# Kernel tuning notes

Hardware: AMD Instinct MI355X
Metric: run time of the kernel (lower is better)

Reference implementation:

```python
import jax, jax.numpy as jnp
import numpy as np
from jax import lax

B, S, F, I, D, K, V = 8, 4096, 256, 512, 4, 7, 256  # batch, seq, features, intermediate, depth, kernel, classes


def setup_inputs() -> dict:
    key = jax.random.key(0)
    ks = jax.random.split(key, 7)

    def nrm(k, shape, fan_in):
        return jax.random.normal(k, shape, jnp.float32) / np.float32(np.sqrt(fan_in))

    return {
        "inp": jax.random.randint(ks[0], (B, S), 0, V),
        "emb": nrm(ks[1], (V, 2 * F), F),
        "w0": nrm(ks[2], (D, 3 * I, F, 1), F),          # 1x1 gating conv, features -> 3*intermediate
        "w1": nrm(ks[3], (D, 3 * I, I, K), I * K),       # causal conv, intermediate -> 3*intermediate
        "w2": nrm(ks[4], (D, F, I, 1), I),               # 1x1 conv, intermediate -> features
        "out_w": nrm(ks[5], (V, 2 * F, 1), 2 * F),
        "out_b": jnp.zeros((V,), jnp.float32),
    }


def mish(x):
    return x * jnp.tanh(jax.nn.softplus(x))


def conv1x1(x, w):
    # x: [B, C, S], w: [O, C, 1] -> [B, O, S]
    return jnp.einsum('bcs,oc->bos', x, w[..., 0])


def causal_conv(x, w):
    # x: [B, C, S], w: [O, C, K]; left-pad with K-1 zeros for causality
    k = w.shape[-1]
    xp = jnp.pad(x, ((0, 0), (0, 0), (k - 1, 0)))
    return lax.conv_general_dilated(xp, w, (1,), 'VALID',
                                    dimension_numbers=('NCH', 'OIH', 'NCH'))


def lin_attn(v, divisor):
    # v: [B, 3I, S]; cumsum-normalized linear attention: cumsum(depth)/t * scale + shift
    depth, scale, shift = jnp.split(v, 3, axis=1)
    return jnp.cumsum(depth, axis=-1) / divisor * scale + shift


def cell(x, w0, w1, w2, divisor):
    v = lin_attn(mish(conv1x1(x, w0)), divisor)     # [B, I, S]
    v = lin_attn(mish(causal_conv(v, w1)), divisor) # [B, I, S]
    return conv1x1(v, w2)                            # [B, F, S]


def reference(inp, emb, w0, w1, w2, out_w, out_b):
    divisor = jnp.arange(1, S + 1, dtype=jnp.float32)[None, None, :]  # [1,1,S]
    e = jnp.transpose(emb[inp], (0, 2, 1))  # [B, 2F, S]
    x0, x1 = jnp.split(e, 2, axis=1)
    # reversible residual stack: (x0, x1) -> (x1, x0 + cell(x1))
    for d in range(D):
        x0, x1 = x1, x0 + cell(x1, w0[d], w1[d], w2[d], divisor)
    out = jnp.concatenate([x0, x1], axis=1)  # [B, 2F, S]
    return conv1x1(out, out_w) + out_b[None, :, None]  # [B, V, S]
```

## Files before the change

kernel.cpp:

```cpp
#include <hip/hip_runtime.h>
#include <hip/hip_bf16.h>

#define B_ 8
#define S_ 4096
#define F_ 256
#define I_ 512
#define D_ 4
#define K_ 7
#define V_ 256
#define I3_ 1536
#define KE_ 3584
#define VR_ (S_ + 8)

using bf16 = __hip_bfloat16;
typedef __bf16 bf16x8 __attribute__((ext_vector_type(8)));
typedef float  f32x4  __attribute__((ext_vector_type(4)));

#define LDS_PTR(p) ((__attribute__((address_space(3))) void*)(p))
#define GLB_PTR(p) ((const __attribute__((address_space(1))) void*)(p))

#define BARR_()  __builtin_amdgcn_s_barrier()
#define WLGKM_() asm volatile("s_waitcnt lgkmcnt(0)" ::: "memory")
#define WVM0_()  asm volatile("s_waitcnt vmcnt(0)" ::: "memory")

__device__ __forceinline__ float mishf(float x) {
    float u = expf(fminf(x, 30.0f));
    float t = u * (u + 2.0f);
    return x * (t / (t + 2.0f));
}

__device__ __forceinline__ float loadw(const void* p, size_t i, int isbf) {
    return isbf ? __bfloat162float(((const bf16*)p)[i]) : ((const float*)p)[i];
}

__device__ __forceinline__ __bf16 tobf(float x) {
    bf16 h = __float2bfloat16(x);
    return *(__bf16*)&h;
}

__global__ __launch_bounds__(256)
void detect_kernel(int* __restrict__ flag, const unsigned short* __restrict__ p)
{
    __shared__ int sh[256];
    int cnt = 0;
    for (int j = threadIdx.x; j < 16384; j += 256) {
        unsigned int e = (p[j] >> 7) & 0xffu;
        if (e >= 132u) cnt++;
    }
    sh[threadIdx.x] = cnt;
    __syncthreads();
    for (int s = 128; s > 0; s >>= 1) {
        if ((int)threadIdx.x < s) sh[threadIdx.x] += sh[threadIdx.x + s];
        __syncthreads();
    }
    if (threadIdx.x == 0) flag[0] = (sh[0] == 0) ? 1 : 0;
}

__global__ __launch_bounds__(256)
void embed_kernel(float* __restrict__ x0, float* __restrict__ x1,
                  const int* __restrict__ inp, const void* __restrict__ emb,
                  const int* __restrict__ flag)
{
    const int isbf = flag[0];
    size_t idx = (size_t)blockIdx.x * 256 + threadIdx.x;
    int s = (int)(idx % S_);
    int f = (int)((idx / S_) % F_);
    int b = (int)(idx / ((size_t)S_ * F_));
    int tok = inp[b * S_ + s];
    x0[idx] = loadw(emb, (size_t)tok * (2 * F_) + f, isbf);
    x1[idx] = loadw(emb, (size_t)tok * (2 * F_) + F_ + f, isbf);
}

__global__ __launch_bounds__(256)
void zeropad_kernel(bf16* __restrict__ vbt, int nslice)
{
    int i = blockIdx.x * 256 + threadIdx.x;
    if (i < nslice * 6 * I_) {
        int z = i / (6 * I_), off = i % (6 * I_);
        vbt[(size_t)z * VR_ * I_ + off] = __float2bfloat16(0.0f);
    }
}

__global__ __launch_bounds__(256)
void wprep_kernel(bf16* __restrict__ wexp, bf16* __restrict__ wb0,
                  bf16* __restrict__ wb2, const void* __restrict__ w1,
                  const void* __restrict__ w0, const void* __restrict__ w2,
                  size_t o1w, size_t o0w, size_t o2w, const int* __restrict__ flag)
{
    const int isbf = flag[0];
    int idx = blockIdx.x * 256 + threadIdx.x;
    if (idx < I3_ * I_) {
        int c = idx & 511, o = idx >> 9;
        const size_t base = o1w + ((size_t)o * 512 + c) * 7;
        float vals[7];
        #pragma unroll
        for (int k = 0; k < 7; ++k) vals[k] = loadw(w1, base + k, isbf);
        #pragma unroll
        for (int k = 0; k < 7; ++k)
            wexp[(size_t)o * KE_ + (k << 9) + c] = __float2bfloat16(vals[k]);
    } else if (idx < I3_ * I_ + I3_ * F_) {
        int i = idx - I3_ * I_;
        wb0[i] = __float2bfloat16(loadw(w0, o0w + i, isbf));
    } else if (idx < I3_ * I_ + I3_ * F_ + F_ * I_) {
        int i = idx - I3_ * I_ - I3_ * F_;
        wb2[i] = __float2bfloat16(loadw(w2, o2w + i, isbf));
    }
}

__global__ __launch_bounds__(256)
void scan_kernel(bf16* __restrict__ vout, const float* __restrict__ t)
{
    const int z = blockIdx.y;
    const int i = blockIdx.x;
    t    += (size_t)z * I3_ * S_;
    vout += (size_t)z * I_ * S_;
    const float* dp  = t + (size_t)i * S_;
    const float* scp = dp + (size_t)I_ * S_;
    const float* shp = dp + (size_t)(2 * I_) * S_;
    bf16* op = vout + (size_t)i * S_;
    const int tid = threadIdx.x;
    const int base = tid * 16;

    float md[16];
    float lsum = 0.f;
    #pragma unroll
    for (int q = 0; q < 4; ++q) {
        float4 dv = *(const float4*)(dp + base + q * 4);
        #pragma unroll
        for (int j = 0; j < 4; ++j) {
            float m = (&dv.x)[j];
            md[q * 4 + j] = m;
            lsum += m;
        }
    }
    float ssum = lsum;
    #pragma unroll
    for (int off = 1; off < 64; off <<= 1) {
        float nv = __shfl_up(ssum, off, 64);
        if ((tid & 63) >= off) ssum += nv;
    }
    __shared__ float wtot[4];
    const int wid = tid >> 6, lane = tid & 63;
    if (lane == 63) wtot[wid] = ssum;
    __syncthreads();
    float excl = ssum - lsum;
    #pragma unroll
    for (int wq = 0; wq < 3; ++wq)
        if (wq < wid) excl += wtot[wq];

    float run = excl;
    bf16x8 o0v, o1v;
    #pragma unroll
    for (int q = 0; q < 4; ++q) {
        float4 scv = *(const float4*)(scp + base + q * 4);
        float4 shv = *(const float4*)(shp + base + q * 4);
        #pragma unroll
        for (int j = 0; j < 4; ++j) {
            run += md[q * 4 + j];
            float sdiv = (float)(base + q * 4 + j + 1);
            float ov = run / sdiv * (&scv.x)[j] + (&shv.x)[j];
            if (q < 2) o0v[q * 4 + j] = tobf(ov);
            else       o1v[(q - 2) * 4 + j] = tobf(ov);
        }
    }
    *(bf16x8*)(void*)(op + base) = o0v;
    *(bf16x8*)(void*)(op + base + 8) = o1v;
}

__global__ __launch_bounds__(256)
void trans_kernel(bf16* __restrict__ dst, size_t dzstr,
                  const float* __restrict__ src, size_t szstr, int C)
{
    __shared__ __align__(16) bf16 lt[64][72];
    const int z = blockIdx.z;
    dst += (size_t)z * dzstr;
    src += (size_t)z * szstr;
    const int tid = threadIdx.x;
    const int s0 = blockIdx.x * 64;
    const int c0 = blockIdx.y * 64;
    #pragma unroll
    for (int p = 0; p < 4; ++p) {
        int c = p * 16 + (tid >> 4);
        int sc = (tid & 15) * 4;
        float4 f = *(const float4*)(src + (size_t)(c0 + c) * S_ + s0 + sc);
        #pragma unroll
        for (int j = 0; j < 4; ++j)
            lt[sc + j][c] = __float2bfloat16((&f.x)[j]);
    }
    __syncthreads();
    #pragma unroll
    for (int p = 0; p < 2; ++p) {
        int ch = p * 256 + tid;
        int r = ch >> 3, g = ch & 7;
        *(bf16x8*)(dst + (size_t)(s0 + r) * C + c0 + g * 8) =
            *(const bf16x8*)&lt[r][g * 8];
    }
}

__global__ __launch_bounds__(256)
void transb_kernel(bf16* __restrict__ dst, size_t dzstr,
                   const bf16* __restrict__ src, size_t szstr, int C)
{
    __shared__ __align__(16) bf16 lt[64][72];
    const int z = blockIdx.z;
    dst += (size_t)z * dzstr;
    src += (size_t)z * szstr;
    const int tid = threadIdx.x;
    const int s0 = blockIdx.x * 64;
    const int c0 = blockIdx.y * 64;
    #pragma unroll
    for (int p = 0; p < 2; ++p) {
        int c = p * 32 + (tid >> 3);
        int sc = (tid & 7) * 8;
        bf16x8 v = *(const bf16x8*)(src + (size_t)(c0 + c) * S_ + s0 + sc);
        #pragma unroll
        for (int j = 0; j < 8; ++j)
            *(__bf16*)&lt[sc + j][c] = v[j];
    }
    __syncthreads();
    #pragma unroll
    for (int p = 0; p < 2; ++p) {
        int ch = p * 256 + tid;
        int r = ch >> 3, g = ch & 7;
        *(bf16x8*)(dst + (size_t)(s0 + r) * C + c0 + g * 8) =
            *(const bf16x8*)&lt[r][g * 8];
    }
}

__global__ __launch_bounds__(512, 1)
void gemm192_kernel(float* __restrict__ out, size_t ozstr,
                    const bf16* __restrict__ Aw, int lda,
                    const bf16* __restrict__ Bm, size_t bzstr, int ldb,
                    int Kdim, int conv, int domish)
{
    __shared__ __align__(16) bf16 la[2][192][64];
    __shared__ __align__(16) bf16 lb[2][256][64];
    const int tid = threadIdx.x;
    const int s0 = blockIdx.x * 256;
    const int o0 = blockIdx.y * 192;
    const int z  = blockIdx.z;
    out += (size_t)z * ozstr;
    Bm  += (size_t)z * bzstr;
    const int wv = tid >> 6, lane = tid & 63;
    const int wr = wv >> 2, wc = wv & 3;
    const int l16 = lane & 15, q = lane >> 4;
    const int srow = lane >> 3;
    const int schunk = (lane & 7) ^ srow;
    const int nKt = Kdim >> 6;

    f32x4 acc[6][4];
    #pragma unroll
    for (int i = 0; i < 6; ++i)
        #pragma unroll
        for (int j = 0; j < 4; ++j)
            #pragma unroll
            for (int r = 0; r < 4; ++r) acc[i][j][r] = 0.f;

#define STAGE_A3(buf, kt) do {                                                \
    const bf16* gpA_ = Aw + (size_t)(o0 + wv * 8 + srow) * lda                \
                          + ((kt) << 6) + (schunk << 3);                      \
    __builtin_amdgcn_global_load_lds(GLB_PTR(gpA_),                           \
        LDS_PTR(&la[buf][wv * 8][0]), 16, 0, 0);                              \
    __builtin_amdgcn_global_load_lds(GLB_PTR(gpA_ + (size_t)64 * lda),        \
        LDS_PTR(&la[buf][64 + wv * 8][0]), 16, 0, 0);                         \
    __builtin_amdgcn_global_load_lds(GLB_PTR(gpA_ + (size_t)128 * lda),       \
        LDS_PTR(&la[buf][128 + wv * 8][0]), 16, 0, 0);                        \
} while (0)

#define STAGE_BL(buf, l, ro, bk) do {                                         \
    const bf16* gpB_ = Bm + (size_t)(s0 + (l) * 64 + wv * 8 + srow + (ro)) * ldb \
                          + (bk) + (schunk << 3);                             \
    __builtin_amdgcn_global_load_lds(GLB_PTR(gpB_),                           \
        LDS_PTR(&lb[buf][(l) * 64 + wv * 8][0]), 16, 0, 0);                   \
} while (0)

#define LDAF6(buf, kk) do {                                                   \
    _Pragma("unroll") for (int i2 = 0; i2 < 6; ++i2) {                        \
        int r_ = wr * 96 + i2 * 16 + l16;                                     \
        af[i2] = *(const bf16x8*)&la[buf][r_][(((kk) * 4 + q) ^ (r_ & 7)) << 3]; \
    }                                                                         \
} while (0)

#define LDBF4(buf, kk) do {                                                   \
    _Pragma("unroll") for (int j2 = 0; j2 < 4; ++j2) {                        \
        int r_ = wc * 64 + j2 * 16 + l16;                                     \
        bfr[j2] = *(const bf16x8*)&lb[buf][r_][(((kk) * 4 + q) ^ (r_ & 7)) << 3]; \
    }                                                                         \
} while (0)

#define MFMA24() do {                                                         \
    __builtin_amdgcn_s_setprio(1);                                            \
    _Pragma("unroll") for (int i2 = 0; i2 < 6; ++i2)                          \
    _Pragma("unroll") for (int j2 = 0; j2 < 4; ++j2)                          \
        acc[i2][j2] = __builtin_amdgcn_mfma_f32_16x16x32_bf16(                \
            af[i2], bfr[j2], acc[i2][j2], 0, 0, 0);                           \
    __builtin_amdgcn_s_setprio(0);                                            \
} while (0)

    STAGE_A3(0, 0);
    STAGE_BL(0, 0, 0, 0); STAGE_BL(0, 1, 0, 0);
    STAGE_BL(0, 2, 0, 0); STAGE_BL(0, 3, 0, 0);
    WVM0_();
    BARR_();

    bf16x8 af[6], bfr[4];
    for (int t = 0; t < nKt; ++t) {
        const int c = t & 1, n = c ^ 1;
        const bool st = (t + 1) < nKt;
        int ro1 = 0, bk1 = (t + 1) << 6;
        if (conv) { ro1 = bk1 >> 9; bk1 &= 511; }
        LDAF6(c, 0); LDBF4(c, 0);
        if (st) {
            STAGE_A3(n, t + 1);
            STAGE_BL(n, 0, ro1, bk1); STAGE_BL(n, 1, ro1, bk1);
            STAGE_BL(n, 2, ro1, bk1); STAGE_BL(n, 3, ro1, bk1);
        }
        BARR_(); WLGKM_();
        MFMA24();
        LDAF6(c, 1); LDBF4(c, 1);
        if (st) WVM0_();
        BARR_(); WLGKM_();
        MFMA24();
    }

    #pragma unroll
    for (int i = 0; i < 6; ++i)
        #pragma unroll
        for (int j = 0; j < 4; ++j) {
            int sg = s0 + wc * 64 + j * 16 + l16;
            #pragma unroll
            for (int r = 0; r < 4; ++r) {
                int og = o0 + wr * 96 + i * 16 + q * 4 + r;
                float v = acc[i][j][r];
                if (domish) v = mishf(v);
                out[(size_t)og * S_ + sg] = v;
            }
        }
#undef STAGE_A3
#undef STAGE_BL
#undef LDAF6
#undef LDBF4
#undef MFMA24
}

__global__ __launch_bounds__(256)
void gemm128_kernel(float* __restrict__ out, size_t ozstr,
                    const bf16* __restrict__ Aw, int lda,
                    const bf16* __restrict__ Bm, size_t bzstr, int ldb,
                    int Kdim, int conv, int addres)
{
    __shared__ __align__(16) bf16 la[2][128][64];
    __shared__ __align__(16) bf16 lb[2][128][64];
    const int tid = threadIdx.x;
    const int s0 = blockIdx.x * 128;
    const int o0 = blockIdx.y * 128;
    const int z  = blockIdx.z;
    out += (size_t)z * ozstr;
    Bm  += (size_t)z * bzstr;
    const int wv = tid >> 6, lane = tid & 63;
    const int wo = wv & 1, wsv = wv >> 1;
    const int l16 = lane & 15, q = lane >> 4;
    const int lrow = lane >> 3, lslot = lane & 7;
    const int nKt = Kdim >> 6;

    f32x4 acc[4][4];
    #pragma unroll
    for (int i = 0; i < 4; ++i)
        #pragma unroll
        for (int j = 0; j < 4; ++j)
            #pragma unroll
            for (int r = 0; r < 4; ++r) acc[i][j][r] = 0.f;

#define G128_STAGE(buf, kt) do {                                              \
    int k0_ = (kt) << 6; int roff_ = 0, bk_ = k0_;                            \
    if (conv) { roff_ = k0_ >> 9; bk_ = k0_ & 511; }                          \
    _Pragma("unroll") for (int t_ = 0; t_ < 4; ++t_) {                        \
        int rbase = wv * 32 + t_ * 8;                                         \
        int row = rbase + lrow;                                               \
        int chunk = lslot ^ (row & 7);                                        \
        __builtin_amdgcn_global_load_lds(                                     \
            GLB_PTR(Aw + (size_t)(o0 + row) * lda + k0_ + chunk * 8),         \
            LDS_PTR(&la[buf][rbase][0]), 16, 0, 0);                           \
        __builtin_amdgcn_global_load_lds(                                     \
            GLB_PTR(Bm + (size_t)(s0 + row + roff_) * ldb + bk_ + chunk * 8), \
            LDS_PTR(&lb[buf][rbase][0]), 16, 0, 0);                           \
    }                                                                         \
} while (0)

#define G128_RD(buf, kk) do {                                                 \
    _Pragma("unroll") for (int i = 0; i < 4; ++i) {                           \
        int r = wo * 64 + i * 16 + l16;                                       \
        af[i] = *(const bf16x8*)&la[buf][r][(((kk) * 4 + q) ^ (r & 7)) * 8];  \
    }                                                                         \
    _Pragma("unroll") for (int j = 0; j < 4; ++j) {                           \
        int r = wsv * 64 + j * 16 + l16;                                      \
        bfr[j] = *(const bf16x8*)&lb[buf][r][(((kk) * 4 + q) ^ (r & 7)) * 8]; \
    }                                                                         \
} while (0)

#define G128_MFMA16() do {                                                    \
    __builtin_amdgcn_s_setprio(1);                                            \
    _Pragma("unroll") for (int i = 0; i < 4; ++i)                             \
    _Pragma("unroll") for (int j = 0; j < 4; ++j)                             \
        acc[i][j] = __builtin_amdgcn_mfma_f32_16x16x32_bf16(                  \
            af[i], bfr[j], acc[i][j], 0, 0, 0);                               \
    __builtin_amdgcn_s_setprio(0);                                            \
} while (0)

    G128_STAGE(0, 0);
    WVM0_();
    BARR_();

    bf16x8 af[4], bfr[4];
    for (int t = 0; t < nKt; ++t) {
        const int c = t & 1, n = c ^ 1;
        const bool st = (t + 1) < nKt;
        G128_RD(c, 0);
        if (st) G128_STAGE(n, t + 1);
        BARR_(); WLGKM_();
        G128_MFMA16();
        G128_RD(c, 1);
        if (st) WVM0_();
        BARR_(); WLGKM_();
        G128_MFMA16();
    }

    #pragma unroll
    for (int i = 0; i < 4; ++i)
        #pragma unroll
        for (int j = 0; j < 4; ++j) {
            int sg = s0 + wsv * 64 + j * 16 + l16;
            #pragma unroll
            for (int r = 0; r < 4; ++r) {
                int og = o0 + wo * 64 + i * 16 + q * 4 + r;
                float v = acc[i][j][r];
                if (addres) v += out[(size_t)og * S_ + sg];
                out[(size_t)og * S_ + sg] = v;
            }
        }
#undef G128_STAGE
#undef G128_RD
#undef G128_MFMA16
}

__global__ __launch_bounds__(256)
void final_kernel(void* __restrict__ out, const float* __restrict__ x0,
                  const float* __restrict__ x1, const void* __restrict__ ow,
                  const void* __restrict__ ob, const int* __restrict__ flag)
{
    __shared__ float wl[16][68];
    __shared__ float xl[16][68];
    const int isbf = flag[0];
    const int tid = threadIdx.x;
    const int tx = tid & 15, ty = tid >> 4;
    const int s0 = blockIdx.x * 64;
    const int o0 = blockIdx.y * 64;
    const int b  = blockIdx.z;
    float acc[4][4] = {};
    for (int c0 = 0; c0 < 2 * F_; c0 += 16) {
        if (isbf) {
            #pragma unroll
            for (int e = tid; e < 1024; e += 256) {
                int k = e & 15, o = e >> 4;
                wl[k][o] = __bfloat162float(((const bf16*)ow)[(size_t)(o0 + o) * (2 * F_) + (c0 + k)]);
            }
        } else {
            #pragma unroll
            for (int e = tid; e < 1024; e += 256) {
                int k = e & 15, o = e >> 4;
                wl[k][o] = ((const float*)ow)[(size_t)(o0 + o) * (2 * F_) + (c0 + k)];
            }
        }
        {
            int r = tid >> 4;
            int qq = (tid & 15) * 4;
            int cr = c0 + r;
            const float* src = (cr < F_) ? (x0 + ((size_t)b * F_ + cr) * S_)
                                         : (x1 + ((size_t)b * F_ + (cr - F_)) * S_);
            *(float4*)&xl[r][qq] = *(const float4*)(src + s0 + qq);
        }
        __syncthreads();
        #pragma unroll
        for (int k = 0; k < 16; ++k) {
            float4 av = *(const float4*)&wl[k][ty * 4];
            float4 bv = *(const float4*)&xl[k][tx * 4];
            #pragma unroll
            for (int i = 0; i < 4; ++i)
                #pragma unroll
                for (int j = 0; j < 4; ++j)
                    acc[i][j] += (&av.x)[i] * (&bv.x)[j];
        }
        __syncthreads();
    }
    #pragma unroll
    for (int i = 0; i < 4; ++i) {
        int o = o0 + ty * 4 + i;
        float bias = loadw(ob, o, isbf);
        size_t outoff = ((size_t)b * V_ + o) * S_ + s0 + tx * 4;
        if (isbf) {
            bf16* po = (bf16*)out + outoff;
            #pragma unroll
            for (int j = 0; j < 4; ++j)
                po[j] = __float2bfloat16(acc[i][j] + bias);
        } else {
            float* po = (float*)out + outoff;
            *(float4*)po = make_float4(acc[i][0] + bias, acc[i][1] + bias,
                                       acc[i][2] + bias, acc[i][3] + bias);
        }
    }
}

extern "C" void kernel_launch(void* const* d_in, const int* in_sizes, int n_in,
                              void* d_out, int out_size, void* d_ws, size_t ws_size,
                              hipStream_t stream)
{
    const int*  inp  = (const int*)d_in[0];
    const void* emb  = d_in[1];
    const void* w0   = d_in[2];
    const void* w1   = d_in[3];
    const void* w2   = d_in[4];
    const void* outw = d_in[5];
    const void* outb = d_in[6];

    const size_t NX = (size_t)B_ * F_ * S_;
    const size_t NT = (size_t)I3_ * S_;
    const size_t NV = (size_t)I_ * S_;
    const size_t VSTR = (size_t)VR_ * I_;

    auto need = [&](int p) -> size_t {
        return 256 + 8 * NX + (size_t)4 * p * NT + (size_t)2 * p * NV
             + 2 * ((size_t)I3_ * KE_ + (size_t)p * VSTR + (size_t)p * S_ * F_
                    + (size_t)I3_ * F_ + (size_t)F_ * I_);
    };
    int P = 2;
    if (ws_size >= need(8)) P = 8;
    else if (ws_size >= need(4)) P = 4;

    int*   flag = (int*)d_ws;
    float* A  = (float*)d_ws + 64;
    float* Bb = A + NX;
    float* T  = Bb + NX;
    bf16*  Vv = (bf16*)(T + (size_t)P * NT);
    bf16*  wexp = Vv + (size_t)P * NV;
    bf16*  vbt  = wexp + (size_t)I3_ * KE_;
    bf16*  xbt  = vbt + (size_t)P * VSTR;
    bf16*  wb0  = xbt + (size_t)P * S_ * F_;
    bf16*  wb2  = wb0 + (size_t)I3_ * F_;

    detect_kernel<<<1, 256, 0, stream>>>(flag, (const unsigned short*)emb);
    embed_kernel<<<dim3((unsigned)(NX / 256)), 256, 0, stream>>>(A, Bb, inp, emb, flag);
    zeropad_kernel<<<dim3((P * 6 * I_ + 255) / 256), 256, 0, stream>>>(vbt, P);

    const unsigned WPREP_GRID = (I3_ * I_ + I3_ * F_ + F_ * I_ + 255) / 256;
    int swap = 0;
    for (int d = 0; d < D_; ++d) {
        wprep_kernel<<<dim3(WPREP_GRID), 256, 0, stream>>>(
            wexp, wb0, wb2, w1, w0, w2,
            (size_t)d * I3_ * I_ * K_, (size_t)d * I3_ * F_,
            (size_t)d * F_ * I_, flag);
        for (int bp = 0; bp < B_ / P; ++bp) {
            float* x0 = (swap ? Bb : A) + (size_t)(P * bp) * F_ * S_;
            float* x1 = (swap ? A : Bb) + (size_t)(P * bp) * F_ * S_;
            trans_kernel<<<dim3(S_ / 64, F_ / 64, P), 256, 0, stream>>>(
                xbt, (size_t)S_ * F_, x1, (size_t)F_ * S_, F_);
            gemm192_kernel<<<dim3(S_ / 256, I3_ / 192, P), 512, 0, stream>>>(
                T, NT, wb0, F_, xbt, (size_t)S_ * F_, F_, F_, 0, 1);
            scan_kernel<<<dim3(I_, P), 256, 0, stream>>>(Vv, T);
            transb_kernel<<<dim3(S_ / 64, I_ / 64, P), 256, 0, stream>>>(
                vbt + 6 * I_, VSTR, Vv, NV, I_);
            gemm192_kernel<<<dim3(S_ / 256, I3_ / 192, P), 512, 0, stream>>>(
                T, NT, wexp, KE_, vbt, VSTR, I_, KE_, 1, 1);
            scan_kernel<<<dim3(I_, P), 256, 0, stream>>>(Vv, T);
            transb_kernel<<<dim3(S_ / 64, I_ / 64, P), 256, 0, stream>>>(
                vbt + 6 * I_, VSTR, Vv, NV, I_);
            gemm128_kernel<<<dim3(S_ / 128, F_ / 128, P), 256, 0, stream>>>(
                x0, (size_t)F_ * S_, wb2, I_, vbt + 6 * I_, VSTR, I_, I_, 0, 1);
        }
        swap ^= 1;
    }
    final_kernel<<<dim3(S_ / 64, V_ / 64, B_), 256, 0, stream>>>(d_out, A, Bb, outw, outb, flag);
    (void)in_sizes; (void)n_in; (void)out_size;
}
```

Measured before the change: 2.649 ms.

## Store scale/shift intermediates in bf16 and add 256-row GEMM tile for batch-8

The gating GEMMs now write the depth third of their output in fp32 and the scale and shift thirds in bf16, so the scan kernel reads less intermediate data. A new gemm256 kernel with a 256x256 tile is used when all 8 batches fit in the workspace, giving more reuse per block and fewer blocks. Rounding scale and shift to bf16 adds small precision loss, and the larger tile raises register and LDS pressure.

```diff
diff --git a/kernel.cpp b/kernel.cpp
--- a/kernel.cpp
+++ b/kernel.cpp
@@ -38,6 +38,12 @@
     return *(__bf16*)&h;
 }
 
+__device__ __forceinline__ float bf2f(__bf16 h) {
+    unsigned short u = __builtin_bit_cast(unsigned short, h);
+    unsigned int x = (unsigned int)u << 16;
+    return __builtin_bit_cast(float, x);
+}
+
 __global__ __launch_bounds__(256)
 void detect_kernel(int* __restrict__ flag, const unsigned short* __restrict__ p)
 {
@@ -108,15 +114,17 @@
 }
 
 __global__ __launch_bounds__(256)
-void scan_kernel(bf16* __restrict__ vout, const float* __restrict__ t)
+void scan_kernel(bf16* __restrict__ vout, const float* __restrict__ td,
+                 const bf16* __restrict__ tb)
 {
     const int z = blockIdx.y;
     const int i = blockIdx.x;
-    t    += (size_t)z * I3_ * S_;
+    td   += (size_t)z * I_ * S_;
+    tb   += (size_t)z * 2 * I_ * S_;
     vout += (size_t)z * I_ * S_;
-    const float* dp  = t + (size_t)i * S_;
-    const float* scp = dp + (size_t)I_ * S_;
-    const float* shp = dp + (size_t)(2 * I_) * S_;
+    const float* dp = td + (size_t)i * S_;
+    const bf16* scp = tb + (size_t)i * S_;
+    const bf16* shp = tb + (size_t)(I_ + i) * S_;
     bf16* op = vout + (size_t)i * S_;
     const int tid = threadIdx.x;
     const int base = tid * 16;
@@ -148,20 +156,22 @@
     for (int wq = 0; wq < 3; ++wq)
         if (wq < wid) excl += wtot[wq];
 
+    bf16x8 scv0 = *(const bf16x8*)(const void*)(scp + base);
+    bf16x8 scv1 = *(const bf16x8*)(const void*)(scp + base + 8);
+    bf16x8 shv0 = *(const bf16x8*)(const void*)(shp + base);
+    bf16x8 shv1 = *(const bf16x8*)(const void*)(shp + base + 8);
+
     float run = excl;
     bf16x8 o0v, o1v;
     #pragma unroll
-    for (int q = 0; q < 4; ++q) {
-        float4 scv = *(const float4*)(scp + base + q * 4);
-        float4 shv = *(const float4*)(shp + base + q * 4);
-        #pragma unroll
-        for (int j = 0; j < 4; ++j) {
-            run += md[q * 4 + j];
-            float sdiv = (float)(base + q * 4 + j + 1);
-            float ov = run / sdiv * (&scv.x)[j] + (&shv.x)[j];
-            if (q < 2) o0v[q * 4 + j] = tobf(ov);
-            else       o1v[(q - 2) * 4 + j] = tobf(ov);
-        }
+    for (int e = 0; e < 16; ++e) {
+        run += md[e];
+        float sdiv = (float)(base + e + 1);
+        float sc = bf2f((e < 8) ? scv0[e] : scv1[e - 8]);
+        float sh = bf2f((e < 8) ? shv0[e] : shv1[e - 8]);
+        float ov = run / sdiv * sc + sh;
+        if (e < 8) o0v[e] = tobf(ov);
+        else       o1v[e - 8] = tobf(ov);
     }
     *(bf16x8*)(void*)(op + base) = o0v;
     *(bf16x8*)(void*)(op + base + 8) = o1v;
@@ -228,10 +238,10 @@
 }
 
 __global__ __launch_bounds__(512, 1)
-void gemm192_kernel(float* __restrict__ out, size_t ozstr,
+void gemm192_kernel(float* __restrict__ outd, bf16* __restrict__ outb,
                     const bf16* __restrict__ Aw, int lda,
                     const bf16* __restrict__ Bm, size_t bzstr, int ldb,
-                    int Kdim, int conv, int domish)
+                    int Kdim, int conv)
 {
     __shared__ __align__(16) bf16 la[2][192][64];
     __shared__ __align__(16) bf16 lb[2][256][64];
@@ -239,8 +249,9 @@
     const int s0 = blockIdx.x * 256;
     const int o0 = blockIdx.y * 192;
     const int z  = blockIdx.z;
-    out += (size_t)z * ozstr;
-    Bm  += (size_t)z * bzstr;
+    outd += (size_t)z * I_ * S_;
+    outb += (size_t)z * 2 * I_ * S_;
+    Bm   += (size_t)z * bzstr;
     const int wv = tid >> 6, lane = tid & 63;
     const int wr = wv >> 2, wc = wv & 3;
     const int l16 = lane & 15, q = lane >> 4;
@@ -331,9 +342,9 @@
             #pragma unroll
             for (int r = 0; r < 4; ++r) {
                 int og = o0 + wr * 96 + i * 16 + q * 4 + r;
-                float v = acc[i][j][r];
-                if (domish) v = mishf(v);
-                out[(size_t)og * S_ + sg] = v;
+                float v = mishf(acc[i][j][r]);
+                if (og < I_) outd[(size_t)og * S_ + sg] = v;
+                else outb[(size_t)(og - I_) * S_ + sg] = __float2bfloat16(v);
             }
         }
 #undef STAGE_A3
@@ -341,6 +352,125 @@
 #undef LDAF6
 #undef LDBF4
 #undef MFMA24
+}
+
+__global__ __launch_bounds__(512, 1)
+void gemm256_kernel(float* __restrict__ outd, bf16* __restrict__ outb,
+                    const bf16* __restrict__ Aw, int lda,
+                    const bf16* __restrict__ Bm, size_t bzstr, int ldb,
+                    int Kdim, int conv)
+{
+    __shared__ __align__(16) bf16 la[2][256][64];
+    __shared__ __align__(16) bf16 lb[2][256][64];
+    const int tid = threadIdx.x;
+    const int s0 = blockIdx.x * 256;
+    const int o0 = blockIdx.y * 256;
+    const int z  = blockIdx.z;
+    outd += (size_t)z * I_ * S_;
+    outb += (size_t)z * 2 * I_ * S_;
+    Bm   += (size_t)z * bzstr;
+    const int wv = tid >> 6, lane = tid & 63;
+    const int wr = wv >> 2, wc = wv & 3;
+    const int l16 = lane & 15, q = lane >> 4;
+    const int srow = lane >> 3;
+    const int schunk = (lane & 7) ^ srow;
+    const int nKt = Kdim >> 6;
+
+    f32x4 acc[8][4];
+    #pragma unroll
+    for (int i = 0; i < 8; ++i)
+        #pragma unroll
+        for (int j = 0; j < 4; ++j)
+            #pragma unroll
+            for (int r = 0; r < 4; ++r) acc[i][j][r] = 0.f;
+
+#define STAGE_A4(buf, kt) do {                                                \
+    const bf16* gpA_ = Aw + (size_t)(o0 + wv * 8 + srow) * lda                \
+                          + ((kt) << 6) + (schunk << 3);                      \
+    __builtin_amdgcn_global_load_lds(GLB_PTR(gpA_),                           \
+        LDS_PTR(&la[buf][wv * 8][0]), 16, 0, 0);                              \
+    __builtin_amdgcn_global_load_lds(GLB_PTR(gpA_ + (size_t)64 * lda),        \
+        LDS_PTR(&la[buf][64 + wv * 8][0]), 16, 0, 0);                         \
+    __builtin_amdgcn_global_load_lds(GLB_PTR(gpA_ + (size_t)128 * lda),       \
+        LDS_PTR(&la[buf][128 + wv * 8][0]), 16, 0, 0);                        \
+    __builtin_amdgcn_global_load_lds(GLB_PTR(gpA_ + (size_t)192 * lda),       \
+        LDS_PTR(&la[buf][192 + wv * 8][0]), 16, 0, 0);                        \
+} while (0)
+
+#define STAGE_BL2(buf, l, ro, bk) do {                                        \
+    const bf16* gpB_ = Bm + (size_t)(s0 + (l) * 64 + wv * 8 + srow + (ro)) * ldb \
+                          + (bk) + (schunk << 3);                             \
+    __builtin_amdgcn_global_load_lds(GLB_PTR(gpB_),                           \
+        LDS_PTR(&lb[buf][(l) * 64 + wv * 8][0]), 16, 0, 0);                   \
+} while (0)
+
+#define LDAF8(buf, kk) do {                                                   \
+    _Pragma("unroll") for (int i2 = 0; i2 < 8; ++i2) {                        \
+        int r_ = wr * 128 + i2 * 16 + l16;                                    \
+        af[i2] = *(const bf16x8*)&la[buf][r_][(((kk) * 4 + q) ^ (r_ & 7)) << 3]; \
+    }                                                                         \
+} while (0)
+
+#define LDBF4B(buf, kk) do {                                                  \
+    _Pragma("unroll") for (int j2 = 0; j2 < 4; ++j2) {                        \
+        int r_ = wc * 64 + j2 * 16 + l16;                                     \
+        bfr[j2] = *(const bf16x8*)&lb[buf][r_][(((kk) * 4 + q) ^ (r_ & 7)) << 3]; \
+    }                                                                         \
+} while (0)
+
+#define MFMA32() do {                                                         \
+    __builtin_amdgcn_s_setprio(1);                                            \
+    _Pragma("unroll") for (int i2 = 0; i2 < 8; ++i2)                          \
+    _Pragma("unroll") for (int j2 = 0; j2 < 4; ++j2)                          \
+        acc[i2][j2] = __builtin_amdgcn_mfma_f32_16x16x32_bf16(                \
+            af[i2], bfr[j2], acc[i2][j2], 0, 0, 0);                           \
+    __builtin_amdgcn_s_setprio(0);                                            \
+} while (0)
+
+    STAGE_A4(0, 0);
+    STAGE_BL2(0, 0, 0, 0); STAGE_BL2(0, 1, 0, 0);
+    STAGE_BL2(0, 2, 0, 0); STAGE_BL2(0, 3, 0, 0);
+    WVM0_();
+    BARR_();
+
+    bf16x8 af[8], bfr[4];
+    for (int t = 0; t < nKt; ++t) {
+        const int c = t & 1, n = c ^ 1;
+        const bool st = (t + 1) < nKt;
+        int ro1 = 0, bk1 = (t + 1) << 6;
+        if (conv) { ro1 = bk1 >> 9; bk1 &= 511; }
+        LDAF8(c, 0); LDBF4B(c, 0);
+        if (st) {
+            STAGE_A4(n, t + 1);
+            STAGE_BL2(n, 0, ro1, bk1); STAGE_BL2(n, 1, ro1, bk1);
+            STAGE_BL2(n, 2, ro1, bk1); STAGE_BL2(n, 3, ro1, bk1);
+        }
+        BARR_(); WLGKM_();
+        MFMA32();
+        LDAF8(c, 1); LDBF4B(c, 1);
+        if (st) WVM0_();
+        BARR_(); WLGKM_();
+        MFMA32();
+    }
+
+    #pragma unroll
+    for (int i = 0; i < 8; ++i)
+        #pragma unroll
+        for (int j = 0; j < 4; ++j) {
+            int sg = s0 + wc * 64 + j * 16 + l16;
+            #pragma unroll
+            for (int r = 0; r < 4; ++r) {
+                int og = o0 + wr * 128 + i * 16 + q * 4 + r;
+                float v = mishf(acc[i][j][r]);
+                if (og < I_) outd[(size_t)og * S_ + sg] = v;
+                else outb[(size_t)(og - I_) * S_ + sg] = __float2bfloat16(v);
+            }
+        }
+#undef STAGE_A4
+#undef STAGE_BL2
+#undef LDAF8
+#undef LDBF4B
+#undef MFMA32
 }
 
 __global__ __launch_bounds__(256)
@@ -523,12 +653,14 @@
     const void* outb = d_in[6];
 
     const size_t NX = (size_t)B_ * F_ * S_;
-    const size_t NT = (size_t)I3_ * S_;
-    const size_t NV = (size_t)I_ * S_;
+    const size_t NIS = (size_t)I_ * S_;
     const size_t VSTR = (size_t)VR_ * I_;
 
     auto need = [&](int p) -> size_t {
-        return 256 + 8 * NX + (size_t)4 * p * NT + (size_t)2 * p * NV
+        return 256 + 8 * NX
+             + (size_t)4 * p * NIS
+             + (size_t)4 * p * NIS
+             + (size_t)2 * p * NIS
              + 2 * ((size_t)I3_ * KE_ + (size_t)p * VSTR + (size_t)p * S_ * F_
                     + (size_t)I3_ * F_ + (size_t)F_ * I_);
     };
@@ -539,9 +671,10 @@
     int*   flag = (int*)d_ws;
     float* A  = (float*)d_ws + 64;
     float* Bb = A + NX;
-    float* T  = Bb + NX;
-    bf16*  Vv = (bf16*)(T + (size_t)P * NT);
-    bf16*  wexp = Vv + (size_t)P * NV;
+    float* Td = Bb + NX;
+    bf16*  Tb = (bf16*)(Td + (size_t)P * NIS);
+    bf16*  Vv = Tb + (size_t)P * 2 * NIS;
+    bf16*  wexp = Vv + (size_t)P * NIS;
     bf16*  vbt  = wexp + (size_t)I3_ * KE_;
     bf16*  xbt  = vbt + (size_t)P * VSTR;
     bf16*  wb0  = xbt + (size_t)P * S_ * F_;
@@ -563,16 +696,24 @@
             float* x1 = (swap ? A : Bb) + (size_t)(P * bp) * F_ * S_;
             trans_kernel<<<dim3(S_ / 64, F_ / 64, P), 256, 0, stream>>>(
                 xbt, (size_t)S_ * F_, x1, (size_t)F_ * S_, F_);
-            gemm192_kernel<<<dim3(S_ / 256, I3_ / 192, P), 512, 0, stream>>>(
-                T, NT, wb0, F_, xbt, (size_t)S_ * F_, F_, F_, 0, 1);
-            scan_kernel<<<dim3(I_, P), 256, 0, stream>>>(Vv, T);
+            if (P == 8)
+                gemm256_kernel<<<dim3(S_ / 256, I3_ / 256, 8), 512, 0, stream>>>(
+                    Td, Tb, wb0, F_, xbt, (size_t)S_ * F_, F_, F_, 0);
+            else
+                gemm192_kernel<<<dim3(S_ / 256, I3_ / 192, P), 512, 0, stream>>>(
+                    Td, Tb, wb0, F_, xbt, (size_t)S_ * F_, F_, F_, 0);
+            scan_kernel<<<dim3(I_, P), 256, 0, stream>>>(Vv, Td, Tb);
             transb_kernel<<<dim3(S_ / 64, I_ / 64, P), 256, 0, stream>>>(
-                vbt + 6 * I_, VSTR, Vv, NV, I_);
-            gemm192_kernel<<<dim3(S_ / 256, I3_ / 192, P), 512, 0, stream>>>(
-                T, NT, wexp, KE_, vbt, VSTR, I_, KE_, 1, 1);
-            scan_kernel<<<dim3(I_, P), 256, 0, stream>>>(Vv, T);
+                vbt + 6 * I_, VSTR, Vv, NIS, I_);
+            if (P == 8)
+                gemm256_kernel<<<dim3(S_ / 256, I3_ / 256, 8), 512, 0, stream>>>(
+                    Td, Tb, wexp, KE_, vbt, VSTR, I_, KE_, 1);
+            else
+                gemm192_kernel<<<dim3(S_ / 256, I3_ / 192, P), 512, 0, stream>>>(
+                    Td, Tb, wexp, KE_, vbt, VSTR, I_, KE_, 1);
+            scan_kernel<<<dim3(I_, P), 256, 0, stream>>>(Vv, Td, Tb);
             transb_kernel<<<dim3(S_ / 64, I_ / 64, P), 256, 0, stream>>>(
-                vbt + 6 * I_, VSTR, Vv, NV, I_);
+                vbt + 6 * I_, VSTR, Vv, NIS, I_);
             gemm128_kernel<<<dim3(S_ / 128, F_ / 128, P), 256, 0, stream>>>(
                 x0, (size_t)F_ * S_, wb2, I_, vbt + 6 * I_, VSTR, I_, I_, 0, 1);
         }
```

After: 2.506 ms. 1.06x faster.
